# Kernel optimization log

Measured on AMD Instinct MI355X. Metric: run time of the kernel, lower is better.

## Reference

```python
import jax, jax.numpy as jnp
import numpy as np

SCALES = (0, 1, 2, 3)
SIGMA_NSQ = 2.0
SIGMA_MAX_INV = 4.0 / (255.0 * 255.0)
GAIN_LIMIT = 100.0  # NEG=False
EPS = 1e-10


def gaussian_kernel_2d(N):
    sigma = N / 5.0
    x = jnp.arange(N, dtype=jnp.float32) - (N - 1) / 2.0
    g = jnp.exp(-(x * x) / (2.0 * sigma * sigma))
    k = jnp.outer(g, g)
    return (k / jnp.sum(k))[None, None]  # [1,1,N,N]


def reflect_pad(x, p):
    return jnp.pad(x, ((0, 0), (0, 0), (p, p), (p, p)), mode='reflect')


def conv2d(x, w, stride=1, groups=1):
    return jax.lax.conv_general_dilated(
        x, w, (stride, stride), 'VALID',
        dimension_numbers=('NCHW', 'OIHW', 'NCHW'),
        feature_group_count=groups)


def vif_num_den(ref, dist):
    ref = ref - 128.0
    dist = dist - 128.0
    h, w = ref.shape[-2], ref.shape[-1]
    nums, dens = [], []
    for scale in SCALES:
        N = 2 ** (4 - scale) + 1
        win = gaussian_kernel_2d(N)
        p = (N - 1) // 2
        if scale > 0:
            h, w = h // 2, w // 2
            ref = conv2d(reflect_pad(ref, p), win, stride=2)[:, :, :h, :w]
            dist = conv2d(reflect_pad(dist, p), win, stride=2)[:, :, :h, :w]
        win5 = jnp.tile(win, (5, 1, 1, 1))  # grouped conv, 5 channels
        inp = jnp.concatenate([ref, dist, ref * ref, dist * dist, ref * dist], axis=1)
        out = conv2d(reflect_pad(inp, p), win5, groups=5)  # [b,5,h,w]
        mu1, mu2, s1, s2, s12 = [out[:, i:i + 1] for i in range(5)]
        s1 = jax.nn.relu(s1 - mu1 * mu1)
        s2 = jax.nn.relu(s2 - mu2 * mu2)
        s12 = s12 - mu1 * mu2
        g = s12 / (s1 + EPS)
        sv = s2 - g * s12
        m1 = s1 < EPS
        g = jnp.where(m1, 0.0, g)
        sv = jnp.where(m1, s2, sv)
        s1 = jnp.where(m1, 0.0, s1)
        m2 = s2 < EPS
        g = jnp.where(m2, 0.0, g)
        sv = jnp.where(m2, 0.0, sv)
        sv = jnp.where(g < 0.0, s2, sv)
        g = jax.nn.relu(g)
        sv = jnp.where(sv <= EPS, EPS, sv)
        g = jnp.minimum(g, GAIN_LIMIT)
        num_ar = jnp.log2(1.0 + g * g * s1 / (sv + SIGMA_NSQ))
        den_ar = jnp.log2(1.0 + s1 / SIGMA_NSQ)
        num_ar = jnp.where(s12 < 0.0, 0.0, num_ar)
        m3 = s1 < SIGMA_NSQ
        num_ar = jnp.where(m3, 1.0 - s2 * SIGMA_MAX_INV, num_ar)
        den_ar = jnp.where(m3, 1.0, den_ar)
        nums.append(jnp.sum(num_ar, axis=(-1, -2, -3)))
        dens.append(jnp.sum(den_ar, axis=(-1, -2, -3)))
    return jnp.stack(nums, axis=-1), jnp.stack(dens, axis=-1)


def setup_inputs() -> dict:
    key = jax.random.key(0)
    k1, k2 = jax.random.split(key)
    shape = (4, 1, 1080, 1920)
    ref = jax.random.uniform(k1, shape, dtype=jnp.float32) * 255.0
    dist = jax.random.uniform(k2, shape, dtype=jnp.float32) * 255.0
    return {"ref": ref, "dist": dist}


def reference(ref, dist):
    num, den = vif_num_den(ref, dist)
    return num / den  # VIF features per scale, shape [b, 4]
```

## Files before the change

kernel.cpp:

```cpp
#include <hip/hip_runtime.h>
#include <math.h>

#define VIF_EPS       1e-10f
#define SIGMA_NSQ     2.0f
#define SIGMA_MAX_INV (4.0f / (255.0f * 255.0f))
#define GAIN_LIMIT    100.0f

typedef float v2f __attribute__((ext_vector_type(2)));
typedef float v4f __attribute__((ext_vector_type(4)));

static __device__ __forceinline__ v2f splat2(float s) {
    v2f v; v.x = s; v.y = s; return v;
}

__device__ __forceinline__ int reflect_idx(int i, int n) {
    i = (i < 0) ? -i : i;
    i = (i >= n) ? (2 * n - 2 - i) : i;
    return i;
}

template <int N>
__device__ __forceinline__ void fill_weights_global(float* gw) {
    const float sigma = (float)N / 5.0f;
    const float denom = 2.0f * sigma * sigma;
    float tmp[N];
    float s = 0.0f;
    for (int i = 0; i < N; ++i) {
        float x = (float)i - (float)(N - 1) * 0.5f;
        float g = expf(-(x * x) / denom);
        tmp[i] = g;
        s += g;
    }
    for (int i = 0; i < N; ++i) gw[i] = tmp[i] / s;
}

__global__ __launch_bounds__(64) void init_weights_kernel(float* __restrict__ gw,
                                                          unsigned* __restrict__ counter) {
    const int tid = threadIdx.x;
    if (tid == 0) fill_weights_global<17>(gw + 0);
    else if (tid == 1) fill_weights_global<9>(gw + 17);
    else if (tid == 2) fill_weights_global<5>(gw + 26);
    else if (tid == 3) fill_weights_global<3>(gw + 31);
    else if (tid == 4) *counter = 0u;
}

__host__ __device__ constexpr int w_off(int N) {
    return (N == 17) ? 0 : (N == 9) ? 17 : (N == 5) ? 26 : 31;
}

constexpr int tile_w(int N) { return (256 - (N - 1)) & ~3; }

template <int N>
struct alignas(16) StatsSmem {
    v2f   a[8][256];
    v2f   bq[8][256];
    float c[8][256];
};
template <int N>
struct alignas(16) DownSmem {
    v2f vb[8][252];
};
struct alignas(16) Stats3Smem {
    union {
        StatsSmem<3> planes;
        v2f vb3[10][481];
    } u2;
    v2f patch[10][240];
};

template <int N, bool FROM_PATCH>
__device__ __forceinline__ void stats_body(
    StatsSmem<N>& sm, const float* __restrict__ refp, const float* __restrict__ distp,
    const v2f* __restrict__ patch,
    const float* __restrict__ gw,
    int h, int w, float shift, double2* __restrict__ partial,
    int sy, int sx, int bx, int b) {
    constexpr int P   = (N - 1) / 2;
    constexpr int TW  = tile_w(N);
    constexpr int TH  = 8;
    constexpr int LR  = TH + 2 * P;
    constexpr int XG4 = TW / 4;
    constexpr int NT  = TH * XG4;
    constexpr int REPS = (NT + 255) / 256;

    const int tid = threadIdx.x;
    const int ytile = bx % sy;
    const int xtile = bx / sy;
    const int x0 = xtile * TW;
    const int y0 = ytile * TH;

    float wr[N];
#pragma unroll
    for (int j = 0; j < N; ++j) wr[j] = gw[j];

    {
        const int cc = tid;
        const int gx = reflect_idx(x0 + cc - P, w);

        v2f accA[TH], accB[TH];
        float accC[TH];
#pragma unroll
        for (int t = 0; t < TH; ++t) {
            accA[t] = splat2(0.f);
            accB[t] = splat2(0.f);
            accC[t] = 0.f;
        }

        auto acc_push = [&](int i, float r, float d) {
            v2f rd; rd.x = r; rd.y = d;
            v2f sq = rd * rd;
            float x = r * d;
#pragma unroll
            for (int t = 0; t < TH; ++t) {
                const int j = i - t;
                if (j >= 0 && j < N) {
                    const float wj = wr[j];
                    accA[t] += splat2(wj) * rd;
                    accB[t] += splat2(wj) * sq;
                    accC[t] += wj * x;
                }
            }
        };

        if constexpr (FROM_PATCH) {
#pragma unroll
            for (int i = 0; i < LR; ++i) {
                v2f pv = patch[i * 240 + gx];
                acc_push(i, pv.x, pv.y);
            }
        } else {
            const float* rbase = refp  + (size_t)b * h * w;
            const float* dbase = distp + (size_t)b * h * w;
            const int rowlo = y0 - P;
            if (rowlo >= 0 && rowlo + LR <= h) {
                unsigned voff = (unsigned)(rowlo * w + gx) * 4u;
                const unsigned vstep = (unsigned)w * 4u;
#pragma unroll
                for (int i = 0; i < LR; ++i) {
                    float r = *(const float*)((const char*)rbase + voff) - shift;
                    float d = *(const float*)((const char*)dbase + voff) - shift;
                    voff += vstep;
                    acc_push(i, r, d);
                }
            } else {
#pragma unroll
                for (int i = 0; i < LR; ++i) {
                    const int gy = reflect_idx(rowlo + i, h);
                    const size_t o = (size_t)gy * w + gx;
                    float r = rbase[o] - shift;
                    float d = dbase[o] - shift;
                    acc_push(i, r, d);
                }
            }
        }
#pragma unroll
        for (int t = 0; t < TH; ++t) {
            sm.a[t][cc]  = accA[t];
            sm.bq[t][cc] = accB[t];
            sm.c[t][cc]  = accC[t];
        }
    }
    __syncthreads();

    float num_v = 0.f, den_v = 0.f;
    {
        constexpr int WC  = N + 3;
        constexpr int F4C = (WC + 3) / 4;
#pragma unroll
        for (int rep = 0; rep < REPS; ++rep) {
            const int task = tid + 256 * rep;
            if (task < NT) {
                const int row = task / XG4;
                const int xg  = task - row * XG4;

                v2f muA[4], muB[4];
                float muC[4];
#pragma unroll
                for (int q = 0; q < 4; ++q) {
                    muA[q] = splat2(0.f);
                    muB[q] = splat2(0.f);
                    muC[q] = 0.f;
                }

                const v4f* A4 = (const v4f*)&sm.a[row][xg * 4];
                const v4f* B4 = (const v4f*)&sm.bq[row][xg * 4];
#pragma unroll
                for (int f = 0; f < WC / 2; ++f) {
                    v4f ta = A4[f];
                    v4f tb = B4[f];
#pragma unroll
                    for (int hlf = 0; hlf < 2; ++hlf) {
                        const int k = 2 * f + hlf;
                        v2f pa = hlf ? __builtin_shufflevector(ta, ta, 2, 3)
                                     : __builtin_shufflevector(ta, ta, 0, 1);
                        v2f pb = hlf ? __builtin_shufflevector(tb, tb, 2, 3)
                                     : __builtin_shufflevector(tb, tb, 0, 1);
#pragma unroll
                        for (int q = 0; q < 4; ++q) {
                            const int j = k - q;
                            if (j >= 0 && j < N) {
                                const float wj = wr[j];
                                muA[q] += splat2(wj) * pa;
                                muB[q] += splat2(wj) * pb;
                            }
                        }
                    }
                }
                {
                    const v4f* C4 = (const v4f*)&sm.c[row][xg * 4];
#pragma unroll
                    for (int f = 0; f < F4C; ++f) {
                        v4f t = C4[f];
#pragma unroll
                        for (int e = 0; e < 4; ++e) {
                            const int k = 4 * f + e;
                            const float x = (e == 0) ? t.x : (e == 1) ? t.y
                                          : (e == 2) ? t.z : t.w;
#pragma unroll
                            for (int q = 0; q < 4; ++q) {
                                const int j = k - q;
                                if (j >= 0 && j < N) muC[q] += wr[j] * x;
                            }
                        }
                    }
                }

                const int gy = y0 + row;
#pragma unroll
                for (int q = 0; q < 4; ++q) {
                    int gx = x0 + xg * 4 + q;
                    if (gx < w && gy < h) {
                        float mu1 = muA[q].x, mu2 = muA[q].y;
                        float s1  = fmaxf(0.f, muB[q].x - mu1 * mu1);
                        float s2  = fmaxf(0.f, muB[q].y - mu2 * mu2);
                        float s12 = muC[q] - mu1 * mu2;

                        float g  = s12 / (s1 + VIF_EPS);
                        float sv = s2 - g * s12;
                        if (s1 < VIF_EPS) { g = 0.f; sv = s2; s1 = 0.f; }
                        if (s2 < VIF_EPS) { g = 0.f; sv = 0.f; }
                        if (g  < 0.f)     { sv = s2; g = 0.f; }
                        if (sv <= VIF_EPS) sv = VIF_EPS;
                        g = fminf(g, GAIN_LIMIT);

                        float num_ar = __log2f(1.f + g * g * s1 / (sv + SIGMA_NSQ));
                        float den_ar = __log2f(1.f + s1 / SIGMA_NSQ);
                        if (s12 < 0.f) num_ar = 0.f;
                        if (s1 < SIGMA_NSQ) { num_ar = 1.f - s2 * SIGMA_MAX_INV; den_ar = 1.f; }
                        num_v += num_ar;
                        den_v += den_ar;
                    }
                }
            }
        }
    }

#pragma unroll
    for (int off = 32; off > 0; off >>= 1) {
        num_v += __shfl_down(num_v, off);
        den_v += __shfl_down(den_v, off);
    }
    __syncthreads();
    float* rs = reinterpret_cast<float*>(&sm);
    const int wid = tid >> 6, lane = tid & 63;
    if (lane == 0) { rs[wid] = num_v; rs[4 + wid] = den_v; }
    __syncthreads();
    if (tid == 0) {
        float ns = rs[0] + rs[1] + rs[2] + rs[3];
        float ds = rs[4] + rs[5] + rs[6] + rs[7];
        partial[(size_t)b * (sy * sx) + bx] = make_double2((double)ns, (double)ds);
    }
}

template <int N>
__device__ __forceinline__ void down_body(
    DownSmem<N>& sm, const float* __restrict__ rin, const float* __restrict__ din,
    const float* __restrict__ gw,
    float* __restrict__ rout, float* __restrict__ dout,
    int h, int w, int h2, int w2, float shift, int dgx, int bx, int b) {
    constexpr int P   = (N - 1) / 2;
    constexpr int TOW = 120, TOH = 8;
    constexpr int IC  = 2 * (TOW - 1) + N;
    constexpr int NR  = 2 * (TOH - 1) + N;
    constexpr int XG4 = TOW / 4;
    constexpr int WL  = N + 6;

    float wr[N];
#pragma unroll
    for (int j = 0; j < N; ++j) wr[j] = gw[j];

    const int tid = threadIdx.x;
    const int xt  = bx % dgx;
    const int yt  = bx / dgx;
    const int x0  = xt * TOW;
    const int y0  = yt * TOH;

    if (tid < IC) {
        const int gx = reflect_idx(2 * x0 - P + tid, w);
        const int rowlo = 2 * y0 - P;
        const float* rbase = rin + (size_t)b * h * w;
        const float* dbase = din + (size_t)b * h * w;

        v2f acc[TOH];
#pragma unroll
        for (int t = 0; t < TOH; ++t) acc[t] = splat2(0.f);

        const bool interior = (rowlo >= 0) && (rowlo + NR <= h);
        if (interior) {
            unsigned voff = (unsigned)(rowlo * w + gx) * 4u;
            const unsigned vstep = (unsigned)w * 4u;
#pragma unroll
            for (int i = 0; i < NR; ++i) {
                v2f x;
                x.x = *(const float*)((const char*)rbase + voff) - shift;
                x.y = *(const float*)((const char*)dbase + voff) - shift;
                voff += vstep;
#pragma unroll
                for (int t = 0; t < TOH; ++t) {
                    const int j = i - 2 * t;
                    if (j >= 0 && j < N) acc[t] += splat2(wr[j]) * x;
                }
            }
        } else {
#pragma unroll
            for (int i = 0; i < NR; ++i) {
                const int gy = reflect_idx(rowlo + i, h);
                const size_t o = (size_t)gy * w + gx;
                v2f x; x.x = rbase[o] - shift; x.y = dbase[o] - shift;
#pragma unroll
                for (int t = 0; t < TOH; ++t) {
                    const int j = i - 2 * t;
                    if (j >= 0 && j < N) acc[t] += splat2(wr[j]) * x;
                }
            }
        }
#pragma unroll
        for (int t = 0; t < TOH; ++t) sm.vb[t][tid] = acc[t];
    }
    __syncthreads();

    if (tid < TOH * XG4) {
        const int row = tid / XG4;
        const int xg  = tid - row * XG4;

        v2f o[4];
#pragma unroll
        for (int q = 0; q < 4; ++q) o[q] = splat2(0.f);

        const v4f* s4 = (const v4f*)&sm.vb[row][8 * xg];
#pragma unroll
        for (int f = 0; f < (WL + 1) / 2; ++f) {
            v4f t = s4[f];
#pragma unroll
            for (int hlf = 0; hlf < 2; ++hlf) {
                const int k = 2 * f + hlf;
                v2f p = hlf ? __builtin_shufflevector(t, t, 2, 3)
                            : __builtin_shufflevector(t, t, 0, 1);
#pragma unroll
                for (int q = 0; q < 4; ++q) {
                    const int j = k - 2 * q;
                    if (j >= 0 && j < N) o[q] += splat2(wr[j]) * p;
                }
            }
        }
        const int gy = y0 + row;
        if (gy < h2) {
            float* rp = rout + (size_t)b * h2 * w2 + (size_t)gy * w2 + x0 + 4 * xg;
            float* dp = dout + (size_t)b * h2 * w2 + (size_t)gy * w2 + x0 + 4 * xg;
            *(float4*)rp = make_float4(o[0].x, o[1].x, o[2].x, o[3].x);
            *(float4*)dp = make_float4(o[0].y, o[1].y, o[2].y, o[3].y);
        }
    }
}

template <int NS, int ND>
__global__ __launch_bounds__(256) void fused_kernel(
    const float* __restrict__ sref, const float* __restrict__ sdist,
    const float* __restrict__ gw,
    int sh, int sw, float sshift, double2* __restrict__ partial, int sy, int sx,
    float* __restrict__ drout, float* __restrict__ ddout,
    int dh2, int dw2, int dgx, int nStats) {
    __shared__ union {
        StatsSmem<NS> s;
        DownSmem<ND>  d;
    } u;
    const int bx = blockIdx.x;
    const int b  = blockIdx.z;
    if (bx < nStats)
        stats_body<NS, false>(u.s, sref, sdist, nullptr, gw + w_off(NS), sh, sw,
                              sshift, partial, sy, sx, bx, b);
    else
        down_body<ND>(u.d, sref, sdist, gw + w_off(ND), drout, ddout,
                      sh, sw, dh2, dw2, sshift, dgx, bx - nStats, b);
}

__device__ __forceinline__ void build_l3_patch(
    v2f* __restrict__ vb3 , v2f* __restrict__ patch ,
    const float* __restrict__ r2, const float* __restrict__ d2,
    const float* __restrict__ gw3, int y0, int b) {
    constexpr int H2v = 270, W2v = 480, H3v = 135;
    const int tid = threadIdx.x;
    const float w0 = gw3[0], w1 = gw3[1], w2 = gw3[2];
    const float* rb = r2 + (size_t)b * H2v * W2v;
    const float* db = d2 + (size_t)b * H2v * W2v;

#pragma unroll
    for (int rep = 0; rep < 2; ++rep) {
        const int t = tid + 256 * rep;
        if (t < 481) {
            const int c2 = reflect_idx(t - 1, W2v);
#pragma unroll
            for (int py = 0; py < 10; ++py) {
                const int y3  = reflect_idx(y0 - 1 + py, H3v);
                const int r0  = reflect_idx(2 * y3 - 1, H2v);
                const int r1  = 2 * y3;
                const int r2i = 2 * y3 + 1;
                v2f m = splat2(0.f);
                v2f x;
                x.x = rb[(size_t)r0 * W2v + c2];  x.y = db[(size_t)r0 * W2v + c2];
                m += splat2(w0) * x;
                x.x = rb[(size_t)r1 * W2v + c2];  x.y = db[(size_t)r1 * W2v + c2];
                m += splat2(w1) * x;
                x.x = rb[(size_t)r2i * W2v + c2]; x.y = db[(size_t)r2i * W2v + c2];
                m += splat2(w2) * x;
                vb3[py * 481 + t] = m;
            }
        }
    }
    __syncthreads();
#pragma unroll
    for (int rep = 0; rep < 10; ++rep) {
        const int idx = tid + 256 * rep;
        if (idx < 2400) {
            const int py = idx / 240;
            const int x3 = idx - py * 240;
            v2f o = splat2(0.f);
            o += splat2(w0) * vb3[py * 481 + 2 * x3 + 0];
            o += splat2(w1) * vb3[py * 481 + 2 * x3 + 1];
            o += splat2(w2) * vb3[py * 481 + 2 * x3 + 2];
            patch[py * 240 + x3] = o;
        }
    }
    __syncthreads();
}

constexpr int RN0 = 1080, RN1 = 272, RN2 = 68, RN3 = 17;
constexpr int RB0 = 0, RB1 = 4 * RN0, RB2 = 4 * (RN0 + RN1), RB3 = 4 * (RN0 + RN1 + RN2);

__global__ __launch_bounds__(256) void level23_kernel(
    const float* __restrict__ ref2, const float* __restrict__ dist2,
    const float* __restrict__ gw,
    double2* __restrict__ p2, double2* __restrict__ p3,
    unsigned* __restrict__ counter,
    const double2* __restrict__ part, float* __restrict__ out) {
    __shared__ union {
        StatsSmem<5> s5;
        Stats3Smem   s3;
    } u;
    __shared__ unsigned slast;
    __shared__ double sn[4], sd[4];

    const int bx  = blockIdx.x;
    const int b   = blockIdx.z;
    const int tid = threadIdx.x;

    if (bx < 68) {
        stats_body<5, false>(u.s5, ref2, dist2, nullptr, gw + w_off(5),
                             270, 480, 0.f, p2, 34, 2, bx, b);
    } else {
        const int bx3 = bx - 68;
        build_l3_patch(&u.s3.u2.vb3[0][0], &u.s3.patch[0][0],
                       ref2, dist2, gw + w_off(3), bx3 * 8, b);
        stats_body<3, true>(u.s3.u2.planes, nullptr, nullptr, &u.s3.patch[0][0],
                            gw + w_off(3), 135, 240, 0.f, p3, 17, 1, bx3, b);
    }

    __threadfence();
    if (tid == 0) {
        const unsigned total = gridDim.x * gridDim.z;
        slast = (atomicAdd(counter, 1u) == total - 1u) ? 1u : 0u;
    }
    __syncthreads();
    if (!slast) return;
    __threadfence();

    const int cntv[4]  = {RN0, RN1, RN2, RN3};
    const int basev[4] = {RB0, RB1, RB2, RB3};
    double accn[16], accd[16];
#pragma unroll
    for (int v = 0; v < 16; ++v) { accn[v] = 0.0; accd[v] = 0.0; }
#pragma unroll
    for (int k = 0; k < 5; ++k) {
#pragma unroll
        for (int v = 0; v < 16; ++v) {
            const int s = v & 3, bb = v >> 2;
            const int i = tid + 256 * k;
            if (i < cntv[s]) {
                double2 t = part[basev[s] + (size_t)bb * cntv[s] + i];
                accn[v] += t.x;
                accd[v] += t.y;
            }
        }
    }
#pragma unroll
    for (int v = 0; v < 16; ++v) {
        double ns = accn[v], ds = accd[v];
#pragma unroll
        for (int off = 32; off > 0; off >>= 1) {
            ns += __shfl_down(ns, off);
            ds += __shfl_down(ds, off);
        }
        const int wid = tid >> 6, lane = tid & 63;
        if (lane == 0) { sn[wid] = ns; sd[wid] = ds; }
        __syncthreads();
        if (tid == 0) {
            double Nv = sn[0] + sn[1] + sn[2] + sn[3];
            double Dv = sd[0] + sd[1] + sd[2] + sd[3];
            out[(v >> 2) * 4 + (v & 3)] = (float)(Nv / Dv);
        }
        __syncthreads();
    }
}

extern "C" void kernel_launch(void* const* d_in, const int* in_sizes, int n_in,
                              void* d_out, int out_size, void* d_ws, size_t ws_size,
                              hipStream_t stream) {
    const float* ref  = (const float*)d_in[0];
    const float* dist = (const float*)d_in[1];
    float* out = (float*)d_out;

    const int B = 4;
    const int H0 = 1080, W0 = 1920;
    const int H1 = 540,  W1 = 960;
    const int H2 = 270,  W2 = 480;

    char*  ws  = (char*)d_ws;
    size_t off = 0;
    auto alloc = [&](size_t bytes) -> void* {
        void* p = ws + off;
        off += (bytes + 255) & ~(size_t)255;
        return p;
    };
    float*    gw      = (float*)alloc(34 * sizeof(float));
    unsigned* counter = (unsigned*)alloc(sizeof(unsigned));
    float* ref1  = (float*)alloc((size_t)B * H1 * W1 * 4);
    float* dist1 = (float*)alloc((size_t)B * H1 * W1 * 4);
    float* ref2  = (float*)alloc((size_t)B * H2 * W2 * 4);
    float* dist2 = (float*)alloc((size_t)B * H2 * W2 * 4);

    const int sx0 = (W0 + tile_w(17) - 1) / tile_w(17), sy0 = (H0 + 7) / 8;
    const int sx1 = (W1 + tile_w(9)  - 1) / tile_w(9),  sy1 = (H1 + 7) / 8;
    const int n0 = sx0 * sy0;
    const int n1 = sx1 * sy1;

    const int dgx1 = W1 / 120, nD1 = dgx1 * ((H1 + 7) / 8);
    const int dgx2 = W2 / 120, nD2 = dgx2 * ((H2 + 7) / 8);

    double2* part = (double2*)alloc((size_t)B * (RN0 + RN1 + RN2 + RN3) * sizeof(double2));
    double2* p0 = part;
    double2* p1 = p0 + (size_t)B * RN0;
    double2* p2 = p1 + (size_t)B * RN1;
    double2* p3 = p2 + (size_t)B * RN2;

    dim3 blk(256);

    init_weights_kernel<<<1, 64, 0, stream>>>(gw, counter);

    fused_kernel<17, 9><<<dim3(n0 + nD1, 1, B), blk, 0, stream>>>(
        ref, dist, gw, H0, W0, 128.0f, p0, sy0, sx0,
        ref1, dist1, H1, W1, dgx1, n0);

    fused_kernel<9, 5><<<dim3(n1 + nD2, 1, B), blk, 0, stream>>>(
        ref1, dist1, gw, H1, W1, 0.0f, p1, sy1, sx1,
        ref2, dist2, H2, W2, dgx2, n1);

    level23_kernel<<<dim3(68 + 17, 1, B), blk, 0, stream>>>(
        ref2, dist2, gw, p2, p3, counter, part, out);
}
```

Before: 204.1 us.

## Batch row loads before convolution and move final reduction to separate kernel

In the stats and downsample passes, all input rows are now loaded into register arrays first and accumulated afterwards, so many loads can be in flight at once instead of being interleaved with FMAs. The last-block atomic counter and in-kernel final reduction are removed from level23_kernel. A new 16-block reduce_kernel sums the per-tile partials, one block per batch and scale. This trades higher register pressure, which may lower occupancy, and one extra kernel launch for more memory-level parallelism and a simpler tail.

```diff
diff --git a/kernel.cpp b/kernel.cpp
--- a/kernel.cpp
+++ b/kernel.cpp
@@ -34,14 +34,12 @@
     for (int i = 0; i < N; ++i) gw[i] = tmp[i] / s;
 }
 
-__global__ __launch_bounds__(64) void init_weights_kernel(float* __restrict__ gw,
-                                                          unsigned* __restrict__ counter) {
+__global__ __launch_bounds__(64) void init_weights_kernel(float* __restrict__ gw) {
     const int tid = threadIdx.x;
     if (tid == 0) fill_weights_global<17>(gw + 0);
     else if (tid == 1) fill_weights_global<9>(gw + 17);
     else if (tid == 2) fill_weights_global<5>(gw + 26);
     else if (tid == 3) fill_weights_global<3>(gw + 31);
-    else if (tid == 4) *counter = 0u;
 }
 
 __host__ __device__ constexpr int w_off(int N) {
@@ -131,27 +129,30 @@
         } else {
             const float* rbase = refp  + (size_t)b * h * w;
             const float* dbase = distp + (size_t)b * h * w;
+
+            float rrow[LR], drow[LR];
             const int rowlo = y0 - P;
             if (rowlo >= 0 && rowlo + LR <= h) {
                 unsigned voff = (unsigned)(rowlo * w + gx) * 4u;
                 const unsigned vstep = (unsigned)w * 4u;
 #pragma unroll
                 for (int i = 0; i < LR; ++i) {
-                    float r = *(const float*)((const char*)rbase + voff) - shift;
-                    float d = *(const float*)((const char*)dbase + voff) - shift;
+                    rrow[i] = *(const float*)((const char*)rbase + voff);
+                    drow[i] = *(const float*)((const char*)dbase + voff);
                     voff += vstep;
-                    acc_push(i, r, d);
                 }
             } else {
 #pragma unroll
                 for (int i = 0; i < LR; ++i) {
                     const int gy = reflect_idx(rowlo + i, h);
                     const size_t o = (size_t)gy * w + gx;
-                    float r = rbase[o] - shift;
-                    float d = dbase[o] - shift;
-                    acc_push(i, r, d);
-                }
-            }
+                    rrow[i] = rbase[o];
+                    drow[i] = dbase[o];
+                }
+            }
+#pragma unroll
+            for (int i = 0; i < LR; ++i)
+                acc_push(i, rrow[i] - shift, drow[i] - shift);
         }
 #pragma unroll
         for (int t = 0; t < TH; ++t) {
@@ -301,37 +302,37 @@
         const float* rbase = rin + (size_t)b * h * w;
         const float* dbase = din + (size_t)b * h * w;
 
-        v2f acc[TOH];
-#pragma unroll
-        for (int t = 0; t < TOH; ++t) acc[t] = splat2(0.f);
-
+        float rr[NR], dd[NR];
         const bool interior = (rowlo >= 0) && (rowlo + NR <= h);
         if (interior) {
             unsigned voff = (unsigned)(rowlo * w + gx) * 4u;
             const unsigned vstep = (unsigned)w * 4u;
 #pragma unroll
             for (int i = 0; i < NR; ++i) {
-                v2f x;
-                x.x = *(const float*)((const char*)rbase + voff) - shift;
-                x.y = *(const float*)((const char*)dbase + voff) - shift;
+                rr[i] = *(const float*)((const char*)rbase + voff);
+                dd[i] = *(const float*)((const char*)dbase + voff);
                 voff += vstep;
-#pragma unroll
-                for (int t = 0; t < TOH; ++t) {
-                    const int j = i - 2 * t;
-                    if (j >= 0 && j < N) acc[t] += splat2(wr[j]) * x;
-                }
             }
         } else {
 #pragma unroll
             for (int i = 0; i < NR; ++i) {
                 const int gy = reflect_idx(rowlo + i, h);
                 const size_t o = (size_t)gy * w + gx;
-                v2f x; x.x = rbase[o] - shift; x.y = dbase[o] - shift;
-#pragma unroll
-                for (int t = 0; t < TOH; ++t) {
-                    const int j = i - 2 * t;
-                    if (j >= 0 && j < N) acc[t] += splat2(wr[j]) * x;
-                }
+                rr[i] = rbase[o];
+                dd[i] = dbase[o];
+            }
+        }
+
+        v2f acc[TOH];
+#pragma unroll
+        for (int t = 0; t < TOH; ++t) acc[t] = splat2(0.f);
+#pragma unroll
+        for (int i = 0; i < NR; ++i) {
+            v2f x; x.x = rr[i] - shift; x.y = dd[i] - shift;
+#pragma unroll
+            for (int t = 0; t < TOH; ++t) {
+                const int j = i - 2 * t;
+                if (j >= 0 && j < N) acc[t] += splat2(wr[j]) * x;
             }
         }
 #pragma unroll
@@ -444,25 +445,16 @@
     __syncthreads();
 }
 
-constexpr int RN0 = 1080, RN1 = 272, RN2 = 68, RN3 = 17;
-constexpr int RB0 = 0, RB1 = 4 * RN0, RB2 = 4 * (RN0 + RN1), RB3 = 4 * (RN0 + RN1 + RN2);
-
 __global__ __launch_bounds__(256) void level23_kernel(
     const float* __restrict__ ref2, const float* __restrict__ dist2,
     const float* __restrict__ gw,
-    double2* __restrict__ p2, double2* __restrict__ p3,
-    unsigned* __restrict__ counter,
-    const double2* __restrict__ part, float* __restrict__ out) {
+    double2* __restrict__ p2, double2* __restrict__ p3) {
     __shared__ union {
         StatsSmem<5> s5;
         Stats3Smem   s3;
     } u;
-    __shared__ unsigned slast;
-    __shared__ double sn[4], sd[4];
-
-    const int bx  = blockIdx.x;
-    const int b   = blockIdx.z;
-    const int tid = threadIdx.x;
+    const int bx = blockIdx.x;
+    const int b  = blockIdx.z;
 
     if (bx < 68) {
         stats_body<5, false>(u.s5, ref2, dist2, nullptr, gw + w_off(5),
@@ -474,51 +466,36 @@
         stats_body<3, true>(u.s3.u2.planes, nullptr, nullptr, &u.s3.patch[0][0],
                             gw + w_off(3), 135, 240, 0.f, p3, 17, 1, bx3, b);
     }
-
-    __threadfence();
-    if (tid == 0) {
-        const unsigned total = gridDim.x * gridDim.z;
-        slast = (atomicAdd(counter, 1u) == total - 1u) ? 1u : 0u;
-    }
-    __syncthreads();
-    if (!slast) return;
-    __threadfence();
-
-    const int cntv[4]  = {RN0, RN1, RN2, RN3};
-    const int basev[4] = {RB0, RB1, RB2, RB3};
-    double accn[16], accd[16];
-#pragma unroll
-    for (int v = 0; v < 16; ++v) { accn[v] = 0.0; accd[v] = 0.0; }
-#pragma unroll
-    for (int k = 0; k < 5; ++k) {
-#pragma unroll
-        for (int v = 0; v < 16; ++v) {
-            const int s = v & 3, bb = v >> 2;
-            const int i = tid + 256 * k;
-            if (i < cntv[s]) {
-                double2 t = part[basev[s] + (size_t)bb * cntv[s] + i];
-                accn[v] += t.x;
-                accd[v] += t.y;
-            }
-        }
-    }
-#pragma unroll
-    for (int v = 0; v < 16; ++v) {
-        double ns = accn[v], ds = accd[v];
-#pragma unroll
-        for (int off = 32; off > 0; off >>= 1) {
-            ns += __shfl_down(ns, off);
-            ds += __shfl_down(ds, off);
-        }
-        const int wid = tid >> 6, lane = tid & 63;
-        if (lane == 0) { sn[wid] = ns; sd[wid] = ds; }
-        __syncthreads();
-        if (tid == 0) {
-            double Nv = sn[0] + sn[1] + sn[2] + sn[3];
-            double Dv = sd[0] + sd[1] + sd[2] + sd[3];
-            out[(v >> 2) * 4 + (v & 3)] = (float)(Nv / Dv);
-        }
-        __syncthreads();
+}
+
+__global__ __launch_bounds__(256) void reduce_kernel(
+    const double2* __restrict__ part, float* __restrict__ out,
+    int4 bases, int4 counts) {
+    __shared__ double sn[4], sd[4];
+    const int s = blockIdx.x & 3;
+    const int b = blockIdx.x >> 2;
+    const int base = (&bases.x)[s];
+    const int cnt  = (&counts.x)[s];
+    const double2* p = part + base + (size_t)b * cnt;
+
+    double ns = 0.0, ds = 0.0;
+    for (int i = threadIdx.x; i < cnt; i += 256) {
+        double2 v = p[i];
+        ns += v.x;
+        ds += v.y;
+    }
+#pragma unroll
+    for (int off = 32; off > 0; off >>= 1) {
+        ns += __shfl_down(ns, off);
+        ds += __shfl_down(ds, off);
+    }
+    const int wid = threadIdx.x >> 6, lane = threadIdx.x & 63;
+    if (lane == 0) { sn[wid] = ns; sd[wid] = ds; }
+    __syncthreads();
+    if (threadIdx.x == 0) {
+        double Nv = sn[0] + sn[1] + sn[2] + sn[3];
+        double Dv = sd[0] + sd[1] + sd[2] + sd[3];
+        out[b * 4 + s] = (float)(Nv / Dv);
     }
 }
 
@@ -541,8 +518,7 @@
         off += (bytes + 255) & ~(size_t)255;
         return p;
     };
-    float*    gw      = (float*)alloc(34 * sizeof(float));
-    unsigned* counter = (unsigned*)alloc(sizeof(unsigned));
+    float* gw    = (float*)alloc(34 * sizeof(float));
     float* ref1  = (float*)alloc((size_t)B * H1 * W1 * 4);
     float* dist1 = (float*)alloc((size_t)B * H1 * W1 * 4);
     float* ref2  = (float*)alloc((size_t)B * H2 * W2 * 4);
@@ -552,19 +528,21 @@
     const int sx1 = (W1 + tile_w(9)  - 1) / tile_w(9),  sy1 = (H1 + 7) / 8;
     const int n0 = sx0 * sy0;
     const int n1 = sx1 * sy1;
+    const int n2 = 68;
+    const int n3 = 17;
 
     const int dgx1 = W1 / 120, nD1 = dgx1 * ((H1 + 7) / 8);
     const int dgx2 = W2 / 120, nD2 = dgx2 * ((H2 + 7) / 8);
 
-    double2* part = (double2*)alloc((size_t)B * (RN0 + RN1 + RN2 + RN3) * sizeof(double2));
+    double2* part = (double2*)alloc((size_t)B * (n0 + n1 + n2 + n3) * sizeof(double2));
     double2* p0 = part;
-    double2* p1 = p0 + (size_t)B * RN0;
-    double2* p2 = p1 + (size_t)B * RN1;
-    double2* p3 = p2 + (size_t)B * RN2;
+    double2* p1 = p0 + (size_t)B * n0;
+    double2* p2 = p1 + (size_t)B * n1;
+    double2* p3 = p2 + (size_t)B * n2;
 
     dim3 blk(256);
 
-    init_weights_kernel<<<1, 64, 0, stream>>>(gw, counter);
+    init_weights_kernel<<<1, 64, 0, stream>>>(gw);
 
     fused_kernel<17, 9><<<dim3(n0 + nD1, 1, B), blk, 0, stream>>>(
         ref, dist, gw, H0, W0, 128.0f, p0, sy0, sx0,
@@ -574,6 +552,11 @@
         ref1, dist1, gw, H1, W1, 0.0f, p1, sy1, sx1,
         ref2, dist2, H2, W2, dgx2, n1);
 
-    level23_kernel<<<dim3(68 + 17, 1, B), blk, 0, stream>>>(
-        ref2, dist2, gw, p2, p3, counter, part, out);
-}
+    level23_kernel<<<dim3(n2 + n3, 1, B), blk, 0, stream>>>(
+        ref2, dist2, gw, p2, p3);
+
+    reduce_kernel<<<16, 256, 0, stream>>>(
+        part, out,
+        make_int4(0, B * n0, B * (n0 + n1), B * (n0 + n1 + n2)),
+        make_int4(n0, n1, n2, n3));
+}
```

Measured after the change: 166.4 us. -18.4%, faster.
